# Kernel optimization log

Hardware: AMD Instinct MI355X
Metric: run time of the kernel (lower is better)

## Reference

```python
import jax, jax.numpy as jnp
import numpy as np

BATCH = 65536
SEQ_LEN = 32
EMB = 64
H = 128


def setup_inputs() -> dict:
    key = jax.random.key(0)
    ks = jax.random.split(key, 12)
    s = 0.05
    inp = {
        "last_pos": jax.random.normal(ks[0], (BATCH, 2), jnp.float32),
        "last_pos_rel": jax.random.normal(ks[1], (BATCH, 2), jnp.float32),
        "hh": jax.random.normal(ks[2], (1, BATCH, H), jnp.float32),
        "ch": jax.random.normal(ks[3], (1, BATCH, H), jnp.float32),
        "seq_start_end": jnp.sort(jax.random.randint(ks[4], (256, 2), 0, BATCH), axis=0),
        # LSTM(embedding_dim -> h_dim), PyTorch gate order [i, f, g, o]
        "w_ih": jax.random.normal(ks[5], (4 * H, EMB), jnp.float32) * s,
        "w_hh": jax.random.normal(ks[6], (4 * H, H), jnp.float32) * s,
        "b_ih": jax.random.normal(ks[7], (4 * H,), jnp.float32) * s,
        "b_hh": jax.random.normal(ks[8], (4 * H,), jnp.float32) * s,
        # spatial_embedding: Linear(2 -> EMB)
        "w_emb": jax.random.normal(ks[9], (EMB, 2), jnp.float32) * s,
        "b_emb": jax.random.normal(ks[10], (EMB,), jnp.float32) * s,
        # hidden2pos: Linear(H -> 2)
        "w_pos": jax.random.normal(ks[11], (2, H), jnp.float32) * s,
        "b_pos": jnp.zeros((2,), jnp.float32),
    }
    return inp


def _decode(last_pos, last_pos_rel, hh, ch, w_ih, w_hh, b_ih, b_hh,
            w_emb, b_emb, w_pos, b_pos):
    h0, c0 = hh[0], ch[0]                      # (B, H)
    x0 = last_pos_rel @ w_emb.T + b_emb        # (B, EMB)
    b = b_ih + b_hh

    def step(carry, _):
        h, c, lp, x = carry
        gates = x @ w_ih.T + h @ w_hh.T + b    # (B, 4H)
        i, f, g, o = jnp.split(gates, 4, axis=-1)
        c2 = jax.nn.sigmoid(f) * c + jax.nn.sigmoid(i) * jnp.tanh(g)
        h2 = jax.nn.sigmoid(o) * jnp.tanh(c2)
        rel = h2 @ w_pos.T + b_pos             # (B, 2)
        cur = rel + lp
        x2 = rel @ w_emb.T + b_emb             # next decoder input embedding
        return (h2, c2, cur, x2), rel

    (hN, cN, _, _), rels = jax.lax.scan(step, (h0, c0, last_pos, x0),
                                        None, length=SEQ_LEN)
    # rels: (SEQ_LEN, B, 2) == pred_traj_fake_rel; hN[None]: (1, B, H)
    return rels, hN[None]


def reference(last_pos, last_pos_rel, hh, ch, seq_start_end,
              w_ih, w_hh, b_ih, b_hh, w_emb, b_emb, w_pos, b_pos):
    # seq_start_end is unused when pool_every_timestep=False
    return _decode(last_pos, last_pos_rel, hh, ch,
                   w_ih, w_hh, b_ih, b_hh, w_emb, b_emb, w_pos, b_pos)
```

## Files before the change

kernel.cpp:

```cpp
#include <hip/hip_runtime.h>

#define B_TOT 65536
#define SEQ   32

typedef __bf16 bf16_8 __attribute__((ext_vector_type(8)));
typedef __bf16 bf16_4 __attribute__((ext_vector_type(4)));
typedef float  float4v __attribute__((ext_vector_type(4)));
typedef float  float2v __attribute__((ext_vector_type(2)));

__device__ inline unsigned short f2bf(float f){
    unsigned u = __builtin_bit_cast(unsigned, f);
    u += 0x7FFFu + ((u >> 16) & 1u);
    return (unsigned short)(u >> 16);
}
__device__ inline float fsig(float x){
    float e = __builtin_amdgcn_exp2f(-1.4426950408889634f * x);
    return __builtin_amdgcn_rcpf(1.0f + e);
}
__device__ inline float ftanh(float x){
    float e = __builtin_amdgcn_exp2f(-2.8853900817779268f * x);
    return 2.0f * __builtin_amdgcn_rcpf(1.0f + e) - 1.0f;
}

__global__ void prep_kernel(const float* __restrict__ w_ih,
                            const float* __restrict__ w_hh,
                            const float* __restrict__ b_ih,
                            const float* __restrict__ b_hh,
                            const float* __restrict__ w_emb,
                            const float* __restrict__ b_emb,
                            const float* __restrict__ w_pos,
                            const float* __restrict__ b_pos,
                            unsigned short* __restrict__ weff,
                            float* __restrict__ beff,
                            float* __restrict__ m2,
                            unsigned short* __restrict__ wposA)
{
    int n = threadIdx.x;
    float m20 = 0.f, m21 = 0.f, bi = 0.f;
    for (int e = 0; e < 64; ++e){
        float wv = w_ih[n*64 + e];
        m20 += w_emb[e*2 + 0] * wv;
        m21 += w_emb[e*2 + 1] * wv;
        bi  += b_emb[e] * wv;
    }
    m2[n]       = m20;
    m2[512 + n] = m21;
    beff[n] = b_ih[n] + b_hh[n] + bi + b_pos[0]*m20 + b_pos[1]*m21;
    for (int k = 0; k < 128; ++k){
        float wv = w_hh[n*128 + k] + w_pos[k]*m20 + w_pos[128 + k]*m21;
        weff[n*128 + k] = f2bf(wv);
    }
    if (n < 256) wposA[n] = f2bf(w_pos[n]);
    for (int idx = n; idx < 14*128; idx += 512) wposA[256 + idx] = 0;
}

__global__ __launch_bounds__(256, 2) void dec_kernel(
    const float* __restrict__ lpr,
    const float* __restrict__ hh,
    const float* __restrict__ ch,
    const float* __restrict__ b_pos,
    const unsigned short* __restrict__ wposA,
    const unsigned short* __restrict__ weff,
    const float* __restrict__ beff,
    const float* __restrict__ m2,
    float* __restrict__ out)
{
    __shared__ __align__(16) unsigned short lh[2][16][136];
    __shared__ float ubuf[16][2];

    const int tid  = threadIdx.x;
    const int w    = tid >> 6;
    const int lane = tid & 63;
    const int q    = lane >> 4;
    const int l    = lane & 15;
    const int row0 = blockIdx.x << 4;
    const int batch = row0 + l;

    bf16_8 wA[8][4];
    float4v bias4[8];
#pragma unroll
    for (int t8 = 0; t8 < 8; ++t8){
        int nbase = ((t8 >> 1) << 7) + 32*w + ((t8 & 1) << 4);
        int gA = nbase + l;
#pragma unroll
        for (int kt = 0; kt < 4; ++kt)
            wA[t8][kt] = *(const bf16_8*)(weff + (gA << 7) + kt*32 + (q << 3));
        bias4[t8] = *(const float4v*)(beff + nbase + (q << 2));
    }

    bf16_8 wpA[4];
#pragma unroll
    for (int kt = 0; kt < 4; ++kt)
        wpA[kt] = *(const bf16_8*)(wposA + (l << 7) + kt*32 + (q << 3));
    const float bp0 = b_pos[0], bp1 = b_pos[1];

    float4v cst[2];
#pragma unroll
    for (int X = 0; X < 2; ++X)
        cst[X] = *(const float4v*)(ch + (batch << 7) + 32*w + 16*X + (q << 2));

    bf16_8 b[4];
#pragma unroll
    for (int kt = 0; kt < 4; ++kt){
        const float* ph = hh + (batch << 7) + kt*32 + (q << 3);
        float4v h0 = *(const float4v*)ph;
        float4v h1 = *(const float4v*)(ph + 4);
        bf16_8 t;
        t[0]=(__bf16)h0[0]; t[1]=(__bf16)h0[1]; t[2]=(__bf16)h0[2]; t[3]=(__bf16)h0[3];
        t[4]=(__bf16)h1[0]; t[5]=(__bf16)h1[1]; t[6]=(__bf16)h1[2]; t[7]=(__bf16)h1[3];
        b[kt] = t;
    }

    if (w == 0){
        float4v r = {0.f, 0.f, 0.f, 0.f};
#pragma unroll
        for (int kt = 0; kt < 4; ++kt)
            r = __builtin_amdgcn_mfma_f32_16x16x32_bf16(wpA[kt], b[kt], r, 0, 0, 0);
        if (q == 0){
            float2v lp = *(const float2v*)(lpr + (batch << 1));
            ubuf[l][0] = lp[0] - (r[0] + bp0);
            ubuf[l][1] = lp[1] - (r[1] + bp1);
        }
    }
    __syncthreads();

    float4v acc[8];

    auto do_gates = [&](){
#pragma unroll
        for (int t8 = 0; t8 < 8; ++t8)
            acc[t8] = __builtin_amdgcn_mfma_f32_16x16x32_bf16(wA[t8][0], b[0], bias4[t8], 0, 0, 0);
#pragma unroll
        for (int kt = 1; kt < 4; ++kt)
#pragma unroll
            for (int t8 = 0; t8 < 8; ++t8)
                acc[t8] = __builtin_amdgcn_mfma_f32_16x16x32_bf16(wA[t8][kt], b[kt], acc[t8], 0, 0, 0);
    };

    auto do_elem_write = [&](int buf, bool finalh){
#pragma unroll
        for (int X = 0; X < 2; ++X){
            bf16_4 hv;
            float4v hf;
#pragma unroll
            for (int r4 = 0; r4 < 4; ++r4){
                float ig = acc[0 + X][r4];
                float fg = acc[2 + X][r4];
                float gg = acc[4 + X][r4];
                float og = acc[6 + X][r4];
                float c2 = fsig(fg)*cst[X][r4] + fsig(ig)*ftanh(gg);
                float h2 = fsig(og)*ftanh(c2);
                cst[X][r4] = c2;
                hv[r4] = (__bf16)h2;
                hf[r4] = h2;
            }
            *(bf16_4*)&lh[buf][l][32*w + 16*X + (q << 2)] = hv;
            if (finalh)
                *(float4v*)(out + SEQ*B_TOT*2 + (batch << 7) + 32*w + 16*X + (q << 2)) = hf;
        }
    };

    auto reload_and_rel = [&](int buf, int t){
#pragma unroll
        for (int kt = 0; kt < 4; ++kt)
            b[kt] = *(const bf16_8*)&lh[buf][l][kt*32 + (q << 3)];
        if (w == (t & 3)){
            float4v r = {0.f, 0.f, 0.f, 0.f};
#pragma unroll
            for (int kt = 0; kt < 4; ++kt)
                r = __builtin_amdgcn_mfma_f32_16x16x32_bf16(wpA[kt], b[kt], r, 0, 0, 0);
            if (q == 0){
                float2v rv;
                rv[0] = r[0] + bp0;
                rv[1] = r[1] + bp1;
                *(float2v*)(out + t*(B_TOT*2) + (batch << 1)) = rv;
            }
        }
    };

    do_gates();
    {
        float u0 = ubuf[l][0], u1 = ubuf[l][1];
#pragma unroll
        for (int t8 = 0; t8 < 8; ++t8){
            int g0 = ((t8 >> 1) << 7) + 32*w + ((t8 & 1) << 4) + (q << 2);
            float4v ma = *(const float4v*)(m2 + g0);
            float4v mb = *(const float4v*)(m2 + 512 + g0);
#pragma unroll
            for (int r4 = 0; r4 < 4; ++r4)
                acc[t8][r4] += u0*ma[r4] + u1*mb[r4];
        }
    }
    do_elem_write(1, false);
    __syncthreads();
    reload_and_rel(1, 0);

    for (int t = 1; t < SEQ; ++t){
        do_gates();
        do_elem_write((t + 1) & 1, t == SEQ - 1);
        __syncthreads();
        reload_and_rel((t + 1) & 1, t);
    }
}

extern "C" void kernel_launch(void* const* d_in, const int* in_sizes, int n_in,
                              void* d_out, int out_size, void* d_ws, size_t ws_size,
                              hipStream_t stream)
{
    (void)in_sizes; (void)n_in; (void)out_size; (void)ws_size;

    const float* lpr   = (const float*)d_in[1];
    const float* hh    = (const float*)d_in[2];
    const float* ch    = (const float*)d_in[3];
    const float* w_ih  = (const float*)d_in[5];
    const float* w_hh  = (const float*)d_in[6];
    const float* b_ih  = (const float*)d_in[7];
    const float* b_hh  = (const float*)d_in[8];
    const float* w_emb = (const float*)d_in[9];
    const float* b_emb = (const float*)d_in[10];
    const float* w_pos = (const float*)d_in[11];
    const float* b_pos = (const float*)d_in[12];

    unsigned short* weff  = (unsigned short*)d_ws;
    float* beff           = (float*)((char*)d_ws + 131072);
    float* m2             = (float*)((char*)d_ws + 131072 + 2048);
    unsigned short* wposA = (unsigned short*)((char*)d_ws + 131072 + 2048 + 4096);

    hipLaunchKernelGGL(prep_kernel, dim3(1), dim3(512), 0, stream,
                       w_ih, w_hh, b_ih, b_hh, w_emb, b_emb, w_pos, b_pos,
                       weff, beff, m2, wposA);
    hipLaunchKernelGGL(dec_kernel, dim3(B_TOT/16), dim3(256), 0, stream,
                       lpr, hh, ch, b_pos, wposA, weff, beff, m2,
                       (float*)d_out);
}
```

Measured before the change: 545.5 us.

## Fold activation scales into weights and merge LSTM gate divisions into shared reciprocals

Pre-scales the gate weights, biases and embedding projection by -log2(e), or -2log2(e) for the g gate, in the prep kernel so the gate accumulators feed exp2 directly. It then rewrites the cell update so c2 needs one reciprocal of a combined denominator and h2 another, instead of five separate sigmoid/tanh reciprocals. This cuts the transcendental and multiply count in the per-step elementwise phase. The final hidden state is also staged through shared memory and written as coalesced contiguous rows. Products of several (1+exp) terms can overflow for large gate magnitudes, and the extra shared buffer raises LDS use.

```diff
diff --git a/kernel.cpp b/kernel.cpp
--- a/kernel.cpp
+++ b/kernel.cpp
@@ -8,18 +8,13 @@
 typedef float  float4v __attribute__((ext_vector_type(4)));
 typedef float  float2v __attribute__((ext_vector_type(2)));
 
+#define SC1 (-1.4426950408889634f)
+#define SC2 (-2.8853900817779268f)
+
 __device__ inline unsigned short f2bf(float f){
     unsigned u = __builtin_bit_cast(unsigned, f);
     u += 0x7FFFu + ((u >> 16) & 1u);
     return (unsigned short)(u >> 16);
-}
-__device__ inline float fsig(float x){
-    float e = __builtin_amdgcn_exp2f(-1.4426950408889634f * x);
-    return __builtin_amdgcn_rcpf(1.0f + e);
-}
-__device__ inline float ftanh(float x){
-    float e = __builtin_amdgcn_exp2f(-2.8853900817779268f * x);
-    return 2.0f * __builtin_amdgcn_rcpf(1.0f + e) - 1.0f;
 }
 
 __global__ void prep_kernel(const float* __restrict__ w_ih,
@@ -43,12 +38,13 @@
         m21 += w_emb[e*2 + 1] * wv;
         bi  += b_emb[e] * wv;
     }
-    m2[n]       = m20;
-    m2[512 + n] = m21;
-    beff[n] = b_ih[n] + b_hh[n] + bi + b_pos[0]*m20 + b_pos[1]*m21;
+    float sc = ((n >> 7) == 2) ? SC2 : SC1;
+    m2[n]       = m20 * sc;
+    m2[512 + n] = m21 * sc;
+    beff[n] = (b_ih[n] + b_hh[n] + bi + b_pos[0]*m20 + b_pos[1]*m21) * sc;
     for (int k = 0; k < 128; ++k){
         float wv = w_hh[n*128 + k] + w_pos[k]*m20 + w_pos[128 + k]*m21;
-        weff[n*128 + k] = f2bf(wv);
+        weff[n*128 + k] = f2bf(wv * sc);
     }
     if (n < 256) wposA[n] = f2bf(w_pos[n]);
     for (int idx = n; idx < 14*128; idx += 512) wposA[256 + idx] = 0;
@@ -67,6 +63,7 @@
 {
     __shared__ __align__(16) unsigned short lh[2][16][136];
     __shared__ float ubuf[16][2];
+    __shared__ __align__(16) float hsh[16][128];
 
     const int tid  = threadIdx.x;
     const int w    = tid >> 6;
@@ -141,22 +138,26 @@
 #pragma unroll
         for (int X = 0; X < 2; ++X){
             bf16_4 hv;
-            float4v hf;
 #pragma unroll
             for (int r4 = 0; r4 < 4; ++r4){
-                float ig = acc[0 + X][r4];
-                float fg = acc[2 + X][r4];
-                float gg = acc[4 + X][r4];
-                float og = acc[6 + X][r4];
-                float c2 = fsig(fg)*cst[X][r4] + fsig(ig)*ftanh(gg);
-                float h2 = fsig(og)*ftanh(c2);
+                float ei = __builtin_amdgcn_exp2f(acc[0 + X][r4]);
+                float ef = __builtin_amdgcn_exp2f(acc[2 + X][r4]);
+                float eg = __builtin_amdgcn_exp2f(acc[4 + X][r4]);
+                float pi_ = 1.f + ei, pf = 1.f + ef;
+                float pg  = 1.f + eg, mg = 1.f - eg;
+                float t2  = pi_ * pg;
+                float den = pf * t2;
+                float num = fmaf(cst[X][r4], t2, pf * mg);
+                float c2  = num * __builtin_amdgcn_rcpf(den);
+                float eo  = __builtin_amdgcn_exp2f(acc[6 + X][r4]);
+                float ec  = __builtin_amdgcn_exp2f(c2 * SC2);
+                float po = 1.f + eo, pc = 1.f + ec, mc = 1.f - ec;
+                float h2 = mc * __builtin_amdgcn_rcpf(po * pc);
                 cst[X][r4] = c2;
                 hv[r4] = (__bf16)h2;
-                hf[r4] = h2;
+                if (finalh) hsh[l][32*w + 16*X + (q << 2) + r4] = h2;
             }
             *(bf16_4*)&lh[buf][l][32*w + 16*X + (q << 2)] = hv;
-            if (finalh)
-                *(float4v*)(out + SEQ*B_TOT*2 + (batch << 7) + 32*w + 16*X + (q << 2)) = hf;
         }
     };
 
@@ -200,6 +201,16 @@
         do_elem_write((t + 1) & 1, t == SEQ - 1);
         __syncthreads();
         reload_and_rel((t + 1) & 1, t);
+    }
+
+    __syncthreads();
+    {
+        int r = tid >> 4, c8 = (tid & 15) << 3;
+        float4v v0 = *(const float4v*)&hsh[r][c8];
+        float4v v1 = *(const float4v*)&hsh[r][c8 + 4];
+        float* po = out + SEQ*B_TOT*2 + ((row0 + r) << 7) + c8;
+        *(float4v*)po = v0;
+        *(float4v*)(po + 4) = v1;
     }
 }
 
```

After: 497.3 us. -8.8%, faster.
